# Optimization experiments

Measured on AMD Instinct MI355X. Metric: run time of the kernel, lower is better.

The kernel has to match this reference:

```python
import jax, jax.numpy as jnp
import numpy as np
from jax import lax

NMS_RADIUS = 4  # module default


def conv2d(x, w, b, pad):
    # x: [B,C,H,W], w: [O,I,kh,kw]
    y = lax.conv_general_dilated(x, w, window_strides=(1, 1),
                                 padding=[(pad, pad), (pad, pad)],
                                 dimension_numbers=('NCHW', 'OIHW', 'NCHW'))
    return y + b[None, :, None, None]


def max_pool(x, r):
    # x: [B,H,W]; kernel (2r+1)x(2r+1), stride 1, pad r (torch pads with -inf)
    k = 2 * r + 1
    return lax.reduce_window(x, -jnp.inf, lax.max,
                             window_dimensions=(1, k, k),
                             window_strides=(1, 1, 1),
                             padding=[(0, 0), (r, r), (r, r)])


def simple_nms(scores, r):
    zeros = jnp.zeros_like(scores)
    max_mask = scores == max_pool(scores, r)
    for _ in range(2):
        supp_mask = max_pool(max_mask.astype(scores.dtype), r) > 0
        supp_scores = jnp.where(supp_mask, zeros, scores)
        new_max_mask = supp_scores == max_pool(supp_scores, r)
        max_mask = max_mask | (new_max_mask & ~supp_mask)
    return jnp.where(max_mask, scores, zeros)


def setup_inputs() -> dict:
    key = jax.random.key(0)
    ks = jax.random.split(key, 7)
    B, Hc, Wc = 16, 60, 80
    x = jax.random.normal(ks[0], (B, 512, Hc, Wc), dtype=jnp.float32)
    wPa = jax.random.normal(ks[1], (256, 512, 3, 3), dtype=jnp.float32) * 0.02
    bPa = jax.random.normal(ks[2], (256,), dtype=jnp.float32) * 0.02
    wPd = jax.random.normal(ks[3], (128, 256, 3, 3), dtype=jnp.float32) * 0.02
    bPd = jax.random.normal(ks[4], (128,), dtype=jnp.float32) * 0.02
    wPg = jax.random.normal(ks[5], (65, 128, 1, 1), dtype=jnp.float32) * 0.02
    bPg = jax.random.normal(ks[6], (65,), dtype=jnp.float32) * 0.02
    return {'x': x, 'wPa': wPa, 'bPa': bPa, 'wPd': wPd, 'bPd': bPd,
            'wPg': wPg, 'bPg': bPg}


def reference(x, wPa, bPa, wPd, bPd, wPg, bPg):
    h1 = jax.nn.relu(conv2d(x, wPa, bPa, pad=1))          # [B,256,Hc,Wc]
    h2 = jax.nn.relu(conv2d(h1, wPd, bPd, pad=1))         # [B,128,Hc,Wc]
    logits = conv2d(h2, wPg, bPg, pad=0)                  # [B,65,Hc,Wc]
    scores = jax.nn.softmax(logits, axis=1)[:, :-1]       # [B,64,Hc,Wc]
    b, _, h, w = scores.shape
    # pixel-unshuffle 8x8 cells -> full resolution
    scores = scores.transpose(0, 2, 3, 1).reshape(b, h, w, 8, 8)
    scores = scores.transpose(0, 1, 3, 2, 4).reshape(b, h * 8, w * 8)
    return simple_nms(scores, NMS_RADIUS)
```

## Files before the change

### kernel.cpp

```cpp
#include <hip/hip_runtime.h>
#include <hip/hip_bf16.h>
#include <math.h>


#define B_      16
#define HC      60
#define WC      80
#define PIX     (HC * WC)
#define HF      480
#define WF      640
#define IMG     (HF * WF)
#define NPIX    (B_ * IMG)

typedef double f64x4 __attribute__((ext_vector_type(4)));

__device__ __forceinline__ int clampi(int v, int lo, int hi) {
    return v < lo ? lo : (v > hi ? hi : v);
}

__global__ __launch_bounds__(256) void cvt_f32_f64(const float* __restrict__ s,
                                                   double* __restrict__ d, int n)
{
    int i = blockIdx.x * 256 + threadIdx.x;
    if (i < n) d[i] = (double)s[i];
}

__global__ __launch_bounds__(256) void prep_w(const float* __restrict__ w,
                                              double* __restrict__ wT,
                                              int CIN, int n)
{
    int i = blockIdx.x * 256 + threadIdx.x;
    if (i >= n) return;
    int cin9 = CIN * 9;
    int oc   = i / cin9;
    int rem  = i - oc * cin9;
    int ic   = rem / 9;
    int dydx = rem - ic * 9;
    size_t dst = ((size_t)((oc >> 4) * (CIN >> 2) + (ic >> 2)) * 9 + dydx) * 64
               + (ic & 3) * 16 + (oc & 15);
    wT[dst] = (double)w[i];
}

template <int CIN, typename TIN, bool RELU>
__global__ __launch_bounds__(256) void conv3x3_mfma(
    const TIN* __restrict__ in,
    const double* __restrict__ wT,
    const double* __restrict__ bias,
    double* __restrict__ out)
{
    const int COUT  = (CIN == 512) ? 256 : 128;
    const int ytile = blockIdx.x;
    const int ocb   = blockIdx.y;
    const int oc0   = ocb * 16;
    const int b     = blockIdx.z;
    const int tid   = threadIdx.x;
    const int wv    = tid >> 6;
    const int lane  = tid & 63;
    const int q     = lane >> 4;
    const int c     = lane & 15;
    const int y0    = ytile * 4;

    in  += (size_t)b * CIN  * PIX;
    out += (size_t)b * COUT * PIX;

    int rowL[4], colL[4];
    {
        f64x4 pr = (f64x4){0.0, 0.0, 0.0, 0.0};
        double a1 = (lane < 16) ? (double)(16 * lane) : 0.0;
        double b1 = (lane < 16) ? 1.0 : 0.0;
        pr = __builtin_amdgcn_mfma_f64_16x16x4f64(a1, b1, pr, 0, 0, 0);
        double a2 = (lane < 16) ? 1.0 : 0.0;
        double b2 = (lane < 16) ? (double)lane : 0.0;
        pr = __builtin_amdgcn_mfma_f64_16x16x4f64(a2, b2, pr, 0, 0, 0);
#pragma unroll
        for (int i = 0; i < 4; ++i) {
            int code = (int)pr[i];
            rowL[i] = (code >> 4) & 15;
            colL[i] = code & 15;
        }
    }

    __shared__ double smem[4 * 6 * 82 + 9 * 64];
    double* act = smem;
    double* wl  = smem + 1968;

    f64x4 acc[5];
#pragma unroll
    for (int t = 0; t < 5; ++t) acc[t] = (f64x4){0.0, 0.0, 0.0, 0.0};

    const int bbase = q * 492 + wv * 82 + c;

    const int NCH = CIN / 4;
    const double* wchunk = wT + (size_t)ocb * NCH * 576;

    for (int chk = 0; chk < NCH; ++chk) {
        __syncthreads();
#pragma unroll
        for (int j = 0; j < 8; ++j) {
            int i = tid + j * 256;
            if (i < 1968) {
                int ick = i / 492;
                int rem = i - ick * 492;
                int ry  = rem / 82;
                int rx  = rem - ry * 82;
                int gy  = y0 - 1 + ry, gx = rx - 1;
                double v = 0.0;
                if ((unsigned)gy < (unsigned)HC && (unsigned)gx < (unsigned)WC)
                    v = (double)in[(size_t)(chk * 4 + ick) * PIX + gy * WC + gx];
                act[i] = v;
            }
        }
        {
            const double* wsrc = wchunk + (size_t)chk * 576;
#pragma unroll
            for (int j = 0; j < 3; ++j) {
                int i = tid + j * 256;
                if (i < 576) wl[i] = wsrc[i];
            }
        }
        __syncthreads();

#pragma unroll
        for (int dy = 0; dy < 3; ++dy) {
#pragma unroll
            for (int dx = 0; dx < 3; ++dx) {
                const int dydx = dy * 3 + dx;
                double a = wl[dydx * 64 + lane];
#pragma unroll
                for (int t = 0; t < 5; ++t) {
                    double bv = act[bbase + dy * 82 + t * 16 + dx];
                    acc[t] = __builtin_amdgcn_mfma_f64_16x16x4f64(a, bv, acc[t], 0, 0, 0);
                }
            }
        }
    }

    const int y = y0 + wv;
#pragma unroll
    for (int t = 0; t < 5; ++t) {
#pragma unroll
        for (int i = 0; i < 4; ++i) {
            const int oc = oc0 + rowL[i];
            double v = acc[t][i] + bias[oc];
            if (RELU) v = fmax(v, 0.0);
            out[(size_t)oc * PIX + y * WC + t * 16 + colL[i]] = v;
        }
    }
}

__global__ __launch_bounds__(256) void conv1x1_softmax_f64(
    const double* __restrict__ h2,
    const double* __restrict__ wg,
    const double* __restrict__ bg,
    double* __restrict__ S)
{
    int p = blockIdx.x * 256 + threadIdx.x;
    if (p >= PIX) return;
    const int b = blockIdx.y;
    const double* h2p = h2 + (size_t)b * 128 * PIX + p;
    double* Sb = S + (size_t)b * IMG;

    double l[65];
#pragma unroll
    for (int o = 0; o < 65; ++o) l[o] = bg[o];

    for (int icc = 0; icc < 128; icc += 8) {
        double h[8];
#pragma unroll
        for (int k = 0; k < 8; ++k) h[k] = h2p[(size_t)(icc + k) * PIX];
#pragma unroll
        for (int o = 0; o < 65; ++o) {
            const double* wp = wg + o * 128 + icc;
            l[o] += h[0] * wp[0] + h[1] * wp[1] + h[2] * wp[2] + h[3] * wp[3]
                  + h[4] * wp[4] + h[5] * wp[5] + h[6] * wp[6] + h[7] * wp[7];
        }
    }

    double m = l[0];
#pragma unroll
    for (int o = 1; o < 65; ++o) m = fmax(m, l[o]);
    double s = 0.0;
#pragma unroll
    for (int o = 0; o < 65; ++o) { l[o] = exp(l[o] - m); s += l[o]; }
    double inv = 1.0 / s;

    int y = p / WC, x = p % WC;
#pragma unroll
    for (int cy = 0; cy < 8; ++cy)
#pragma unroll
        for (int cx2 = 0; cx2 < 8; ++cx2)
            Sb[(y * 8 + cy) * WF + x * 8 + cx2] = l[cy * 8 + cx2] * inv;
}

__global__ __launch_bounds__(256) void hmax9_f64(const double* __restrict__ in,
                                                 double* __restrict__ out)
{
    int p = blockIdx.x * 256 + threadIdx.x;
    int x = p % WF;
    const double* row = in + (p - x);
    double m = row[x];
#pragma unroll
    for (int d = 1; d <= 4; ++d) {
        m = fmax(m, row[clampi(x - d, 0, WF - 1)]);
        m = fmax(m, row[clampi(x + d, 0, WF - 1)]);
    }
    out[p] = m;
}

__global__ __launch_bounds__(256) void vmax9_eq(const double* __restrict__ T,
                                                const double* __restrict__ S,
                                                unsigned char* __restrict__ M)
{
    int p = blockIdx.x * 256 + threadIdx.x;
    int y = (p % IMG) / WF;
    double m = T[p];
#pragma unroll
    for (int d = 1; d <= 4; ++d) {
        m = fmax(m, T[p + (clampi(y - d, 0, HF - 1) - y) * WF]);
        m = fmax(m, T[p + (clampi(y + d, 0, HF - 1) - y) * WF]);
    }
    M[p] = (S[p] == m) ? (unsigned char)1 : (unsigned char)0;
}

__global__ __launch_bounds__(256) void hor9_u8(const unsigned char* __restrict__ in,
                                               unsigned char* __restrict__ out)
{
    int p = blockIdx.x * 256 + threadIdx.x;
    int x = p % WF;
    const unsigned char* row = in + (p - x);
    unsigned char m = row[x];
#pragma unroll
    for (int d = 1; d <= 4; ++d) {
        m = m | row[clampi(x - d, 0, WF - 1)];
        m = m | row[clampi(x + d, 0, WF - 1)];
    }
    out[p] = m;
}

__global__ __launch_bounds__(256) void vor9_sup(const unsigned char* __restrict__ T8,
                                                unsigned char* __restrict__ SUP)
{
    int p = blockIdx.x * 256 + threadIdx.x;
    int y = (p % IMG) / WF;
    unsigned char m = T8[p];
#pragma unroll
    for (int d = 1; d <= 4; ++d) {
        m = m | T8[p + (clampi(y - d, 0, HF - 1) - y) * WF];
        m = m | T8[p + (clampi(y + d, 0, HF - 1) - y) * WF];
    }
    SUP[p] = m;
}

__global__ __launch_bounds__(256) void hmax9_supp(const double* __restrict__ S,
                                                  const unsigned char* __restrict__ SUP,
                                                  double* __restrict__ T)
{
    int p = blockIdx.x * 256 + threadIdx.x;
    int x = p % WF;
    int base = p - x;
    double m = SUP[p] ? 0.0 : S[p];
#pragma unroll
    for (int d = 1; d <= 4; ++d) {
        int i1 = base + clampi(x - d, 0, WF - 1);
        int i2 = base + clampi(x + d, 0, WF - 1);
        m = fmax(m, SUP[i1] ? 0.0 : S[i1]);
        m = fmax(m, SUP[i2] ? 0.0 : S[i2]);
    }
    T[p] = m;
}

__global__ __launch_bounds__(256) void vmax9_newmask(const double* __restrict__ T,
                                                     const double* __restrict__ S,
                                                     const unsigned char* __restrict__ SUP,
                                                     unsigned char* __restrict__ M)
{
    int p = blockIdx.x * 256 + threadIdx.x;
    int y = (p % IMG) / WF;
    double m = T[p];
#pragma unroll
    for (int d = 1; d <= 4; ++d) {
        m = fmax(m, T[p + (clampi(y - d, 0, HF - 1) - y) * WF]);
        m = fmax(m, T[p + (clampi(y + d, 0, HF - 1) - y) * WF]);
    }
    unsigned char nw = (!SUP[p] && S[p] == m) ? 1 : 0;
    M[p] = M[p] | nw;
}

__global__ __launch_bounds__(256) void final_mask(const double* __restrict__ S,
                                                  const unsigned char* __restrict__ M,
                                                  float* __restrict__ out)
{
    int p = blockIdx.x * 256 + threadIdx.x;
    out[p] = M[p] ? (float)S[p] : 0.f;
}

extern "C" void kernel_launch(void* const* d_in, const int* in_sizes, int n_in,
                              void* d_out, int out_size, void* d_ws, size_t ws_size,
                              hipStream_t stream)
{
    const float* x   = (const float*)d_in[0];
    const float* wPa = (const float*)d_in[1];
    const float* bPa = (const float*)d_in[2];
    const float* wPd = (const float*)d_in[3];
    const float* bPd = (const float*)d_in[4];
    const float* wPg = (const float*)d_in[5];
    const float* bPg = (const float*)d_in[6];
    float* out = (float*)d_out;

    char* ws = (char*)d_ws;
    double*        S   = (double*)(ws);
    double*        T   = (double*)(ws + 39321600);
    unsigned char* M   = (unsigned char*)(ws + 78643200);
    unsigned char* SUP = (unsigned char*)(ws + 83558400);
    unsigned char* T8  = (unsigned char*)(ws + 88473600);
    double* w1t = (double*)(ws + 39321600);
    double* w2t = (double*)(ws + 48758784);
    double* wgd = (double*)(ws + 51118080);
    double* b1d = (double*)(ws + 51184640);
    double* b2d = (double*)(ws + 51186688);
    double* bgd = (double*)(ws + 51187712);
    char*   hbase = ws + 51188736;

    int G = 1;
    for (int g = 16; g >= 1; g >>= 1) {
        if ((size_t)51188736 + (size_t)g * 14745600 <= ws_size) { G = g; break; }
    }

    prep_w<<<(1179648 + 255) / 256, 256, 0, stream>>>(wPa, w1t, 512, 1179648);
    prep_w<<<(294912 + 255) / 256, 256, 0, stream>>>(wPd, w2t, 256, 294912);
    cvt_f32_f64<<<(8320 + 255) / 256, 256, 0, stream>>>(wPg, wgd, 8320);
    cvt_f32_f64<<<1, 256, 0, stream>>>(bPa, b1d, 256);
    cvt_f32_f64<<<1, 256, 0, stream>>>(bPd, b2d, 128);
    cvt_f32_f64<<<1, 256, 0, stream>>>(bPg, bgd, 65);

    for (int bg0 = 0; bg0 < B_; bg0 += G) {
        int Gc = (bg0 + G <= B_) ? G : (B_ - bg0);
        double* h1s = (double*)hbase;
        double* h2s = (double*)(hbase + (size_t)G * 9830400);
        const float* xb = x + (size_t)bg0 * 512 * PIX;
        conv3x3_mfma<512, float, true><<<dim3(15, 16, Gc), 256, 0, stream>>>(xb, w1t, b1d, h1s);
        conv3x3_mfma<256, double, true><<<dim3(15, 8, Gc), 256, 0, stream>>>(h1s, w2t, b2d, h2s);
        conv1x1_softmax_f64<<<dim3(19, Gc), 256, 0, stream>>>(h2s, wgd, bgd, S + (size_t)bg0 * IMG);
    }

    const int NB = NPIX / 256;
    hmax9_f64<<<NB, 256, 0, stream>>>(S, T);
    vmax9_eq<<<NB, 256, 0, stream>>>(T, S, M);
    for (int it = 0; it < 2; ++it) {
        hor9_u8<<<NB, 256, 0, stream>>>(M, T8);
        vor9_sup<<<NB, 256, 0, stream>>>(T8, SUP);
        hmax9_supp<<<NB, 256, 0, stream>>>(S, SUP, T);
        vmax9_newmask<<<NB, 256, 0, stream>>>(T, S, SUP, M);
    }
    final_mask<<<NB, 256, 0, stream>>>(S, M, out);
}
```

Measured before the change: 5.427 ms.

## Double-buffer conv3x3 chunks via registers and compute two OC blocks per workgroup

The 3x3 convolution kernel now prefetches the next input-channel chunk (activations and weights) into registers while MFMAs run on the current shared-memory buffer, then stores into a second LDS buffer. Each workgroup also computes 32 output channels instead of 16, so every activation tile loaded from global memory feeds twice as many MFMAs, and the grid's y dimension is halved. The cost is more registers (doubled accumulators plus prefetch registers) and more LDS per block, which may reduce occupancy, along with fewer blocks in flight.

```diff
diff --git a/kernel.cpp b/kernel.cpp
--- a/kernel.cpp
+++ b/kernel.cpp
@@ -49,9 +49,9 @@
     double* __restrict__ out)
 {
     const int COUT  = (CIN == 512) ? 256 : 128;
+    const int NCH   = CIN / 4;
     const int ytile = blockIdx.x;
-    const int ocb   = blockIdx.y;
-    const int oc0   = ocb * 16;
+    const int ocp   = blockIdx.y;
     const int b     = blockIdx.z;
     const int tid   = threadIdx.x;
     const int wv    = tid >> 6;
@@ -80,70 +80,113 @@
         }
     }
 
-    __shared__ double smem[4 * 6 * 82 + 9 * 64];
-    double* act = smem;
-    double* wl  = smem + 1968;
-
-    f64x4 acc[5];
-#pragma unroll
-    for (int t = 0; t < 5; ++t) acc[t] = (f64x4){0.0, 0.0, 0.0, 0.0};
+    __shared__ double smem[2][3120];
+
+    const double* wbase = wT + (size_t)(ocp * 2) * NCH * 576;
+
+    f64x4 acc[2][5];
+#pragma unroll
+    for (int o = 0; o < 2; ++o)
+#pragma unroll
+        for (int t = 0; t < 5; ++t) acc[o][t] = (f64x4){0.0, 0.0, 0.0, 0.0};
 
     const int bbase = q * 492 + wv * 82 + c;
 
-    const int NCH = CIN / 4;
-    const double* wchunk = wT + (size_t)ocb * NCH * 576;
+    double ra[8];
+    double rw[5];
+
+#define LOAD_CHUNK(chk)                                                        \
+    {                                                                          \
+        const int ch = (chk);                                                  \
+        _Pragma("unroll")                                                      \
+        for (int j = 0; j < 8; ++j) {                                          \
+            int i = tid + j * 256;                                             \
+            if (i < 1968) {                                                    \
+                int ick = i / 492;                                             \
+                int rem = i - ick * 492;                                       \
+                int ry  = rem / 82;                                            \
+                int rx  = rem - ry * 82;                                       \
+                int gy  = y0 - 1 + ry, gx = rx - 1;                            \
+                double v = 0.0;                                                \
+                if ((unsigned)gy < (unsigned)HC && (unsigned)gx < (unsigned)WC)\
+                    v = (double)in[(size_t)(ch * 4 + ick) * PIX + gy * WC + gx];\
+                ra[j] = v;                                                     \
+            }                                                                  \
+        }                                                                      \
+        _Pragma("unroll")                                                      \
+        for (int j = 0; j < 5; ++j) {                                          \
+            int i = tid + j * 256;                                             \
+            if (i < 1152) {                                                    \
+                int o   = i / 576;                                             \
+                int rem = i - o * 576;                                         \
+                rw[j] = wbase[((size_t)o * NCH + ch) * 576 + rem];             \
+            }                                                                  \
+        }                                                                      \
+    }
+
+#define STORE_CHUNK(buf)                                                       \
+    {                                                                          \
+        double* dst = (buf);                                                   \
+        _Pragma("unroll")                                                      \
+        for (int j = 0; j < 8; ++j) {                                          \
+            int i = tid + j * 256;                                             \
+            if (i < 1968) dst[i] = ra[j];                                      \
+        }                                                                      \
+        _Pragma("unroll")                                                      \
+        for (int j = 0; j < 5; ++j) {                                          \
+            int i = tid + j * 256;                                             \
+            if (i < 1152) dst[1968 + i] = rw[j];                               \
+        }                                                                      \
+    }
+
+    LOAD_CHUNK(0);
+    STORE_CHUNK(smem[0]);
+    __syncthreads();
 
     for (int chk = 0; chk < NCH; ++chk) {
-        __syncthreads();
-#pragma unroll
-        for (int j = 0; j < 8; ++j) {
-            int i = tid + j * 256;
-            if (i < 1968) {
-                int ick = i / 492;
-                int rem = i - ick * 492;
-                int ry  = rem / 82;
-                int rx  = rem - ry * 82;
-                int gy  = y0 - 1 + ry, gx = rx - 1;
-                double v = 0.0;
-                if ((unsigned)gy < (unsigned)HC && (unsigned)gx < (unsigned)WC)
-                    v = (double)in[(size_t)(chk * 4 + ick) * PIX + gy * WC + gx];
-                act[i] = v;
-            }
-        }
-        {
-            const double* wsrc = wchunk + (size_t)chk * 576;
-#pragma unroll
-            for (int j = 0; j < 3; ++j) {
-                int i = tid + j * 256;
-                if (i < 576) wl[i] = wsrc[i];
-            }
-        }
-        __syncthreads();
+        const int cur = chk & 1;
+        if (chk + 1 < NCH) LOAD_CHUNK(chk + 1);
+
+        const double* act = smem[cur];
+        const double* wl  = smem[cur] + 1968;
 
 #pragma unroll
         for (int dy = 0; dy < 3; ++dy) {
 #pragma unroll
             for (int dx = 0; dx < 3; ++dx) {
                 const int dydx = dy * 3 + dx;
-                double a = wl[dydx * 64 + lane];
+                double a0 = wl[dydx * 64 + lane];
+                double a1 = wl[576 + dydx * 64 + lane];
 #pragma unroll
                 for (int t = 0; t < 5; ++t) {
                     double bv = act[bbase + dy * 82 + t * 16 + dx];
-                    acc[t] = __builtin_amdgcn_mfma_f64_16x16x4f64(a, bv, acc[t], 0, 0, 0);
+                    acc[0][t] = __builtin_amdgcn_mfma_f64_16x16x4f64(a0, bv, acc[0][t], 0, 0, 0);
+                    acc[1][t] = __builtin_amdgcn_mfma_f64_16x16x4f64(a1, bv, acc[1][t], 0, 0, 0);
                 }
             }
         }
-    }
+
+        __syncthreads();
+        if (chk + 1 < NCH) {
+            STORE_CHUNK(smem[cur ^ 1]);
+            __syncthreads();
+        }
+    }
+#undef LOAD_CHUNK
+#undef STORE_CHUNK
 
     const int y = y0 + wv;
 #pragma unroll
-    for (int t = 0; t < 5; ++t) {
-#pragma unroll
-        for (int i = 0; i < 4; ++i) {
-            const int oc = oc0 + rowL[i];
-            double v = acc[t][i] + bias[oc];
-            if (RELU) v = fmax(v, 0.0);
-            out[(size_t)oc * PIX + y * WC + t * 16 + colL[i]] = v;
+    for (int o = 0; o < 2; ++o) {
+#pragma unroll
+        for (int t = 0; t < 5; ++t) {
+#pragma unroll
+            for (int i = 0; i < 4; ++i) {
+                const int oc = ocp * 32 + o * 16 + rowL[i];
+                double v = acc[o][t][i] + bias[oc];
+                if (RELU) v = fmax(v, 0.0);
+                out[(size_t)oc * PIX + y * WC + t * 16 + colL[i]] = v;
+            }
         }
     }
 }
@@ -338,8 +381,8 @@
         double* h1s = (double*)hbase;
         double* h2s = (double*)(hbase + (size_t)G * 9830400);
         const float* xb = x + (size_t)bg0 * 512 * PIX;
-        conv3x3_mfma<512, float, true><<<dim3(15, 16, Gc), 256, 0, stream>>>(xb, w1t, b1d, h1s);
-        conv3x3_mfma<256, double, true><<<dim3(15, 8, Gc), 256, 0, stream>>>(h1s, w2t, b2d, h2s);
+        conv3x3_mfma<512, float, true><<<dim3(15, 8, Gc), 256, 0, stream>>>(xb, w1t, b1d, h1s);
+        conv3x3_mfma<256, double, true><<<dim3(15, 4, Gc), 256, 0, stream>>>(h1s, w2t, b2d, h2s);
         conv1x1_softmax_f64<<<dim3(19, Gc), 256, 0, stream>>>(h2s, wgd, bgd, S + (size_t)bg0 * IMG);
     }
 
```

Result: no change. 5.332 ms (-1.8%).

## Double-buffer conv3x3 shared tiles with register prefetch two chunks ahead

Applied to the files above, without the earlier changes.

The 3x3 FP64 MFMA conv kernel now uses two shared-memory buffers and stages the next input/weight chunk through registers. Loads for chunk+2 are issued while chunk computes and chunk+1 is stored to the alternate buffer, leaving one barrier per iteration instead of two. Gather offsets are precomputed once per thread, and launch bounds request 4 blocks per CU. The cost is doubled LDS use (about 40KB per block) and extra registers, which may limit occupancy.

```diff
diff --git a/kernel.cpp b/kernel.cpp
--- a/kernel.cpp
+++ b/kernel.cpp
@@ -42,13 +42,14 @@
 }
 
 template <int CIN, typename TIN, bool RELU>
-__global__ __launch_bounds__(256) void conv3x3_mfma(
+__global__ __launch_bounds__(256, 4) void conv3x3_mfma(
     const TIN* __restrict__ in,
     const double* __restrict__ wT,
     const double* __restrict__ bias,
     double* __restrict__ out)
 {
     const int COUT  = (CIN == 512) ? 256 : 128;
+    const int NCH   = CIN / 4;
     const int ytile = blockIdx.x;
     const int ocb   = blockIdx.y;
     const int oc0   = ocb * 16;
@@ -80,9 +81,9 @@
         }
     }
 
-    __shared__ double smem[4 * 6 * 82 + 9 * 64];
-    double* act = smem;
-    double* wl  = smem + 1968;
+    __shared__ double smem[2][2544];
+
+    const double* wchunk = wT + (size_t)ocb * NCH * 576;
 
     f64x4 acc[5];
 #pragma unroll
@@ -90,42 +91,62 @@
 
     const int bbase = q * 492 + wv * 82 + c;
 
-    const int NCH = CIN / 4;
-    const double* wchunk = wT + (size_t)ocb * NCH * 576;
+    int aOff[8];
+#pragma unroll
+    for (int j = 0; j < 8; ++j) {
+        int i   = tid + j * 256;
+        int ick = i / 492;
+        int rem = i - ick * 492;
+        int ry  = rem / 82;
+        int rx  = rem - ry * 82;
+        int gy  = y0 - 1 + ry, gx = rx - 1;
+        bool ok = (i < 1968) && ((unsigned)gy < (unsigned)HC) && ((unsigned)gx < (unsigned)WC);
+        aOff[j] = ok ? (ick * PIX + gy * WC + gx) : -1;
+    }
+
+    double ra[8];
+    double rw0, rw1, rw2;
+
+#define LOADC(ch)                                                              \
+    {                                                                          \
+        const int gbase = (ch) * 4 * PIX;                                      \
+        _Pragma("unroll")                                                      \
+        for (int j = 0; j < 8; ++j)                                            \
+            ra[j] = (aOff[j] >= 0) ? (double)in[gbase + aOff[j]] : 0.0;        \
+        const double* wp = wchunk + (size_t)(ch) * 576;                        \
+        rw0 = wp[tid];                                                         \
+        rw1 = wp[256 + tid];                                                   \
+        rw2 = (tid < 64) ? wp[512 + tid] : 0.0;                                \
+    }
+
+#define STOREC(sel)                                                            \
+    {                                                                          \
+        double* dst = smem[sel];                                               \
+        _Pragma("unroll")                                                      \
+        for (int j = 0; j < 7; ++j) dst[tid + j * 256] = ra[j];                \
+        if (tid < 176) dst[tid + 1792] = ra[7];                                \
+        dst[1968 + tid] = rw0;                                                 \
+        dst[1968 + 256 + tid] = rw1;                                           \
+        if (tid < 64) dst[1968 + 512 + tid] = rw2;                             \
+    }
+
+    LOADC(0);
+    STOREC(0);
+    LOADC(1);
+    __syncthreads();
 
     for (int chk = 0; chk < NCH; ++chk) {
-        __syncthreads();
-#pragma unroll
-        for (int j = 0; j < 8; ++j) {
-            int i = tid + j * 256;
-            if (i < 1968) {
-                int ick = i / 492;
-                int rem = i - ick * 492;
-                int ry  = rem / 82;
-                int rx  = rem - ry * 82;
-                int gy  = y0 - 1 + ry, gx = rx - 1;
-                double v = 0.0;
-                if ((unsigned)gy < (unsigned)HC && (unsigned)gx < (unsigned)WC)
-                    v = (double)in[(size_t)(chk * 4 + ick) * PIX + gy * WC + gx];
-                act[i] = v;
-            }
-        }
-        {
-            const double* wsrc = wchunk + (size_t)chk * 576;
-#pragma unroll
-            for (int j = 0; j < 3; ++j) {
-                int i = tid + j * 256;
-                if (i < 576) wl[i] = wsrc[i];
-            }
-        }
-        __syncthreads();
-
+        const int cur = chk & 1;
+        if (chk + 1 < NCH) STOREC(cur ^ 1);
+        if (chk + 2 < NCH) LOADC(chk + 2);
+
+        const double* act = smem[cur];
+        const double* wl  = smem[cur] + 1968;
 #pragma unroll
         for (int dy = 0; dy < 3; ++dy) {
 #pragma unroll
             for (int dx = 0; dx < 3; ++dx) {
-                const int dydx = dy * 3 + dx;
-                double a = wl[dydx * 64 + lane];
+                double a = wl[(dy * 3 + dx) * 64 + lane];
 #pragma unroll
                 for (int t = 0; t < 5; ++t) {
                     double bv = act[bbase + dy * 82 + t * 16 + dx];
@@ -133,7 +154,10 @@
                 }
             }
         }
-    }
+        if (chk + 1 < NCH) __syncthreads();
+    }
+#undef LOADC
+#undef STOREC
 
     const int y = y0 + wv;
 #pragma unroll
```

New measurement: 4.782 ms. 11.9% less time.
